# Kernel tuning notes

Hardware: AMD Instinct MI355X
Metric: run time of the kernel (lower is better)

## Reference

```python
import jax, jax.numpy as jnp
import numpy as np

B, T, H, DFF = 32, 4096, 512, 512  # hidden_size=512, d_ff=512, h feature dim = 2*H


def setup_inputs() -> dict:
    key = jax.random.key(0)
    ks = jax.random.split(key, 8)
    sc = 0.02
    return {
        "s": jax.random.normal(ks[0], (B, H), dtype=jnp.float32),
        "h": jax.random.normal(ks[1], (B, T, 2 * H), dtype=jnp.float32),
        "W_a_w": jax.random.normal(ks[2], (DFF, H), dtype=jnp.float32) * sc,
        "W_a_b": jnp.zeros((DFF,), dtype=jnp.float32),
        "U_a_w": jax.random.normal(ks[3], (DFF, 2 * H), dtype=jnp.float32) * sc,
        "U_a_b": jnp.zeros((DFF,), dtype=jnp.float32),
        "V_a_w": jax.random.normal(ks[4], (1, DFF), dtype=jnp.float32) * sc,
        "V_a_b": jnp.zeros((1,), dtype=jnp.float32),
    }


def reference(s, h, W_a_w, W_a_b, U_a_w, U_a_b, V_a_w, V_a_b):
    # Bahdanau additive attention scoring (NOTE: original has no softmax).
    ws = s @ W_a_w.T + W_a_b                              # [B, d_ff]
    uh = jnp.einsum('bte,fe->btf', h, U_a_w) + U_a_b       # [B, T, d_ff]
    x = jnp.tanh(ws[:, None, :] + uh)                      # [B, T, d_ff]
    energy = x @ V_a_w[0] + V_a_b[0]                       # [B, T]
    context = jnp.einsum('bt,bte->be', energy, h)          # [B, 2*hidden]
    return context
```

## Files before the change

kernel.cpp:

```cpp
#include <hip/hip_runtime.h>
#include <cstdint>
#include <cstddef>

#define B_SZ 32
#define T_SZ 4096
#define H2   1024
#define DFF_ 512
#define TM   64
#define NCHUNK 16
#define NSTEP 32

typedef __attribute__((ext_vector_type(8))) short bf16x8;
typedef __attribute__((ext_vector_type(4))) float f32x4;
typedef __attribute__((ext_vector_type(8))) unsigned short u16x8;

__device__ __forceinline__ unsigned short f2bf(float x) {
  unsigned u = __float_as_uint(x);
  u += 0x7fffu + ((u >> 16) & 1u);
  return (unsigned short)(u >> 16);
}

__device__ __forceinline__ void gll16(const float* g, void* l) {
  __builtin_amdgcn_global_load_lds(
      (const __attribute__((address_space(1))) unsigned int*)g,
      (__attribute__((address_space(3))) unsigned int*)l, 16, 0, 0);
}

__device__ __forceinline__ void memfence_sched() { asm volatile("" ::: "memory"); }

__device__ __forceinline__ void blk_barrier() {
  asm volatile("" ::: "memory");
  __builtin_amdgcn_s_barrier();
  asm volatile("" ::: "memory");
}

__global__ void prep_u_kernel(const float* __restrict__ U,
                              unsigned short* __restrict__ Upk) {
  int g = blockIdx.x * 256 + threadIdx.x;
  int j  = g & 7;
  int l  = (g >> 3) & 63;
  int ct = (g >> 9) & 31;
  int ks = g >> 14;
  int f  = ct * 16 + (l & 15);
  int k  = ks * 32 + (l >> 4) * 8 + j;
  Upk[g] = f2bf(U[f * H2 + k]);
}

__global__ void prep_ws_kernel(const float* __restrict__ s, const float* __restrict__ W,
                               const float* __restrict__ Wb, const float* __restrict__ Ub,
                               float* __restrict__ wsm) {
  int idx = blockIdx.x * 256 + threadIdx.x;
  int b = idx >> 9, f = idx & 511;
  const float4* s4 = (const float4*)(s + b * 512);
  const float4* w4 = (const float4*)(W + f * 512);
  float acc = 0.f;
  #pragma unroll 4
  for (int i = 0; i < 128; ++i) {
    float4 a = s4[i], w = w4[i];
    acc += a.x * w.x + a.y * w.y + a.z * w.z + a.w * w.w;
  }
  wsm[idx] = acc + Wb[f] + Ub[f];
}

__global__ __launch_bounds__(512, 4) void attn_main(
    const float* __restrict__ h, const unsigned short* __restrict__ Upk,
    const float* __restrict__ wsm, const float* __restrict__ Vw,
    const float* __restrict__ Vb, float* __restrict__ out) {
  __shared__ float F32c[2][4096];
  __shared__ unsigned short As16[2][4096];
  __shared__ float ws_s[DFF_];
  __shared__ float V_s[DFF_];
  __shared__ float energy_part[8][TM];
  __shared__ float energy_s[TM];

  const int tid  = threadIdx.x;
  const int blk  = blockIdx.x;
  const int b    = blk >> 6;
  const int t0   = (blk & 63) * TM;
  const int lane = tid & 63;
  const int wave = tid >> 6;
  const int ln15 = lane & 15;
  const int q4   = lane >> 4;

  ws_s[tid] = wsm[b * DFF_ + tid];
  V_s[tid]  = Vw[tid];

  const float* hbase = h + ((size_t)(b * T_SZ + t0)) * H2;

  const float* gsrc = hbase + (size_t)(8 * wave + (lane >> 4)) * H2 + (lane & 15) * 4;

  const int crow = 8 * wave + (lane >> 3);
  const int ckg  = lane & 7;
  const int cread  = crow * 64 + ckg * 8;
  const int cwrite = (ckg >> 2) * 2048 + (crow >> 4) * 512
                   + ((ckg & 3) * 16 + (crow & 15)) * 8;

  const bf16x8* Upk8 = (const bf16x8*)Upk;

  f32x4 acc[16];
  #pragma unroll
  for (int i = 0; i < 16; ++i) acc[i] = (f32x4){0.f, 0.f, 0.f, 0.f};
  bf16x8 bcur[8];

  gll16(gsrc,            (char*)&F32c[0][0] + wave * 2048);
  gll16(gsrc + 4 * H2,   (char*)&F32c[0][0] + wave * 2048 + 1024);
  memfence_sched();
  #pragma unroll
  for (int st = 0; st < 2; ++st)
    #pragma unroll
    for (int i = 0; i < 4; ++i)
      bcur[st * 4 + i] = Upk8[(size_t)(st * 32 + wave * 4 + i) * 64 + lane];
  memfence_sched();
  gll16(gsrc + 64,          (char*)&F32c[1][0] + wave * 2048);
  gll16(gsrc + 64 + 4 * H2, (char*)&F32c[1][0] + wave * 2048 + 1024);
  asm volatile("s_waitcnt vmcnt(10)" ::: "memory");
  {
    const float* src = &F32c[0][cread];
    float4 x0 = *(const float4*)src;
    float4 x1 = *(const float4*)(src + 4);
    u16x8 o;
    o[0] = f2bf(x0.x); o[1] = f2bf(x0.y); o[2] = f2bf(x0.z); o[3] = f2bf(x0.w);
    o[4] = f2bf(x1.x); o[5] = f2bf(x1.y); o[6] = f2bf(x1.z); o[7] = f2bf(x1.w);
    *(u16x8*)&As16[0][cwrite] = o;
  }
  blk_barrier();

  for (int c = 0; c < NCHUNK; ++c) {
    const unsigned short* Ab = &As16[c & 1][0];
    #pragma unroll
    for (int st = 0; st < 2; ++st) {
      #pragma unroll
      for (int rt = 0; rt < 4; ++rt) {
        bf16x8 af = *(const bf16x8*)&Ab[st * 2048 + rt * 512 + lane * 8];
        #pragma unroll
        for (int ct2 = 0; ct2 < 4; ++ct2)
          acc[ct2 * 4 + rt] =
            __builtin_amdgcn_mfma_f32_16x16x32_bf16(af, bcur[st * 4 + ct2],
                                                    acc[ct2 * 4 + rt], 0, 0, 0);
      }
    }
    if (c < NCHUNK - 1) {
      asm volatile("s_waitcnt vmcnt(0)" ::: "memory");
      {
        const float* src = &F32c[(c + 1) & 1][cread];
        float4 x0 = *(const float4*)src;
        float4 x1 = *(const float4*)(src + 4);
        u16x8 o;
        o[0] = f2bf(x0.x); o[1] = f2bf(x0.y); o[2] = f2bf(x0.z); o[3] = f2bf(x0.w);
        o[4] = f2bf(x1.x); o[5] = f2bf(x1.y); o[6] = f2bf(x1.z); o[7] = f2bf(x1.w);
        *(u16x8*)&As16[(c + 1) & 1][cwrite] = o;
      }
      blk_barrier();
      const int g0 = (c + 1) * 2;
      #pragma unroll
      for (int st = 0; st < 2; ++st)
        #pragma unroll
        for (int i = 0; i < 4; ++i)
          bcur[st * 4 + i] = Upk8[(size_t)((g0 + st) * 32 + wave * 4 + i) * 64 + lane];
      memfence_sched();
      if (c < NCHUNK - 2) {
        const float* gs = gsrc + (c + 2) * 64;
        char* ld = (char*)&F32c[c & 1][0] + wave * 2048;
        gll16(gs,          ld);
        gll16(gs + 4 * H2, ld + 1024);
      }
    }
  }

  float esum[16];
  #pragma unroll
  for (int i = 0; i < 16; ++i) esum[i] = 0.f;
  #pragma unroll
  for (int ct2 = 0; ct2 < 4; ++ct2) {
    int f = wave * 64 + ct2 * 16 + ln15;
    float wsf = ws_s[f], vf = V_s[f];
    #pragma unroll
    for (int rt = 0; rt < 4; ++rt) {
      #pragma unroll
      for (int rg = 0; rg < 4; ++rg) {
        float z = wsf + acc[ct2 * 4 + rt][rg];
        float e = __expf(2.f * z);
        float x = 1.f - 2.f / (e + 1.f);
        esum[rt * 4 + rg] += x * vf;
      }
    }
  }
  #pragma unroll
  for (int i = 0; i < 16; ++i) {
    #pragma unroll
    for (int m = 1; m < 16; m <<= 1) esum[i] += __shfl_xor(esum[i], m, 64);
  }
  if (ln15 == 0) {
    #pragma unroll
    for (int rt = 0; rt < 4; ++rt)
      #pragma unroll
      for (int rg = 0; rg < 4; ++rg)
        energy_part[wave][rt * 16 + q4 * 4 + rg] = esum[rt * 4 + rg];
  }
  __syncthreads();
  if (tid < TM) {
    float e = Vb[0];
    #pragma unroll
    for (int w = 0; w < 8; ++w) e += energy_part[w][tid];
    energy_s[tid] = e;
  }
  __syncthreads();

  int e0 = tid * 2;
  float c0 = 0.f, c1 = 0.f;
  const float2* h2p = (const float2*)hbase + (e0 >> 1);
  #pragma unroll 8
  for (int row = 0; row < TM; ++row) {
    float en = energy_s[row];
    float2 hv = h2p[(size_t)row * (H2 / 2)];
    c0 += en * hv.x;
    c1 += en * hv.y;
  }
  atomicAdd(&out[b * H2 + e0], c0);
  atomicAdd(&out[b * H2 + e0 + 1], c1);
}

extern "C" void kernel_launch(void* const* d_in, const int* in_sizes, int n_in,
                              void* d_out, int out_size, void* d_ws, size_t ws_size,
                              hipStream_t stream) {
  const float* s  = (const float*)d_in[0];
  const float* h  = (const float*)d_in[1];
  const float* Ww = (const float*)d_in[2];
  const float* Wb = (const float*)d_in[3];
  const float* Uw = (const float*)d_in[4];
  const float* Ub = (const float*)d_in[5];
  const float* Vw = (const float*)d_in[6];
  const float* Vb = (const float*)d_in[7];
  float* out = (float*)d_out;

  unsigned short* Upk = (unsigned short*)d_ws;
  float* wsm = (float*)((char*)d_ws + (size_t)NSTEP * 32768);

  hipMemsetAsync(out, 0, (size_t)out_size * sizeof(float), stream);
  prep_u_kernel<<<(DFF_ * H2) / 256, 256, 0, stream>>>(Uw, Upk);
  prep_ws_kernel<<<(B_SZ * DFF_) / 256, 256, 0, stream>>>(s, Ww, Wb, Ub, wsm);
  attn_main<<<B_SZ * (T_SZ / TM), 512, 0, stream>>>(h, Upk, wsm, Vw, Vb, out);
}
```

Measured before the change: 866.5 us.

## Triple-buffer h staging, reorder convert before MFMA, swizzle bf16 LDS tile

```diff
diff --git a/kernel.cpp b/kernel.cpp
--- a/kernel.cpp
+++ b/kernel.cpp
@@ -27,12 +27,6 @@
 }
 
 __device__ __forceinline__ void memfence_sched() { asm volatile("" ::: "memory"); }
-
-__device__ __forceinline__ void blk_barrier() {
-  asm volatile("" ::: "memory");
-  __builtin_amdgcn_s_barrier();
-  asm volatile("" ::: "memory");
-}
 
 __global__ void prep_u_kernel(const float* __restrict__ U,
                               unsigned short* __restrict__ Upk) {
@@ -66,7 +60,7 @@
     const float* __restrict__ h, const unsigned short* __restrict__ Upk,
     const float* __restrict__ wsm, const float* __restrict__ Vw,
     const float* __restrict__ Vb, float* __restrict__ out) {
-  __shared__ float F32c[2][4096];
+  __shared__ float F32c[3][4096];
   __shared__ unsigned short As16[2][4096];
   __shared__ float ws_s[DFF_];
   __shared__ float V_s[DFF_];
@@ -91,9 +85,11 @@
 
   const int crow = 8 * wave + (lane >> 3);
   const int ckg  = lane & 7;
-  const int cread  = crow * 64 + ckg * 8;
-  const int cwrite = (ckg >> 2) * 2048 + (crow >> 4) * 512
-                   + ((ckg & 3) * 16 + (crow & 15)) * 8;
+  const int cread = crow * 64 + ckg * 8;
+  int cwq = (ckg & 3) * 16 + (crow & 15);
+  cwq ^= (cwq >> 4) & 3;
+  const int cwrite = (ckg >> 2) * 2048 + (crow >> 4) * 512 + cwq * 8;
+  const int lrd = (lane ^ ((lane >> 4) & 3)) * 8;
 
   const bf16x8* Upk8 = (const bf16x8*)Upk;
 
@@ -102,8 +98,17 @@
   for (int i = 0; i < 16; ++i) acc[i] = (f32x4){0.f, 0.f, 0.f, 0.f};
   bf16x8 bcur[8];
 
-  gll16(gsrc,            (char*)&F32c[0][0] + wave * 2048);
-  gll16(gsrc + 4 * H2,   (char*)&F32c[0][0] + wave * 2048 + 1024);
+  {
+    char* lb = (char*)&F32c[0][0] + wave * 2048;
+    gll16(gsrc,          lb);
+    gll16(gsrc + 4 * H2, lb + 1024);
+    lb = (char*)&F32c[1][0] + wave * 2048;
+    gll16(gsrc + 64,          lb);
+    gll16(gsrc + 64 + 4 * H2, lb + 1024);
+    lb = (char*)&F32c[2][0] + wave * 2048;
+    gll16(gsrc + 128,          lb);
+    gll16(gsrc + 128 + 4 * H2, lb + 1024);
+  }
   memfence_sched();
   #pragma unroll
   for (int st = 0; st < 2; ++st)
@@ -111,9 +116,7 @@
     for (int i = 0; i < 4; ++i)
       bcur[st * 4 + i] = Upk8[(size_t)(st * 32 + wave * 4 + i) * 64 + lane];
   memfence_sched();
-  gll16(gsrc + 64,          (char*)&F32c[1][0] + wave * 2048);
-  gll16(gsrc + 64 + 4 * H2, (char*)&F32c[1][0] + wave * 2048 + 1024);
-  asm volatile("s_waitcnt vmcnt(10)" ::: "memory");
+  asm volatile("s_waitcnt vmcnt(12)" ::: "memory");
   {
     const float* src = &F32c[0][cread];
     float4 x0 = *(const float4*)src;
@@ -123,26 +126,18 @@
     o[4] = f2bf(x1.x); o[5] = f2bf(x1.y); o[6] = f2bf(x1.z); o[7] = f2bf(x1.w);
     *(u16x8*)&As16[0][cwrite] = o;
   }
-  blk_barrier();
-
+  asm volatile("s_waitcnt lgkmcnt(0)" ::: "memory");
+  __builtin_amdgcn_s_barrier();
+  memfence_sched();
+
+  int s0 = 0;
   for (int c = 0; c < NCHUNK; ++c) {
-    const unsigned short* Ab = &As16[c & 1][0];
-    #pragma unroll
-    for (int st = 0; st < 2; ++st) {
-      #pragma unroll
-      for (int rt = 0; rt < 4; ++rt) {
-        bf16x8 af = *(const bf16x8*)&Ab[st * 2048 + rt * 512 + lane * 8];
-        #pragma unroll
-        for (int ct2 = 0; ct2 < 4; ++ct2)
-          acc[ct2 * 4 + rt] =
-            __builtin_amdgcn_mfma_f32_16x16x32_bf16(af, bcur[st * 4 + ct2],
-                                                    acc[ct2 * 4 + rt], 0, 0, 0);
-      }
-    }
+    int s1 = s0 + 1; if (s1 == 3) s1 = 0;
     if (c < NCHUNK - 1) {
-      asm volatile("s_waitcnt vmcnt(0)" ::: "memory");
+      if (c < NCHUNK - 2) { asm volatile("s_waitcnt vmcnt(10)" ::: "memory"); }
+      else                { asm volatile("s_waitcnt vmcnt(8)"  ::: "memory"); }
       {
-        const float* src = &F32c[(c + 1) & 1][cread];
+        const float* src = &F32c[s1][cread];
         float4 x0 = *(const float4*)src;
         float4 x1 = *(const float4*)(src + 4);
         u16x8 o;
@@ -150,21 +145,39 @@
         o[4] = f2bf(x1.x); o[5] = f2bf(x1.y); o[6] = f2bf(x1.z); o[7] = f2bf(x1.w);
         *(u16x8*)&As16[(c + 1) & 1][cwrite] = o;
       }
-      blk_barrier();
+      if (c <= NCHUNK - 4) {
+        const float* gs = gsrc + (size_t)(c + 3) * 64;
+        char* lb = (char*)&F32c[s0][0] + wave * 2048;
+        gll16(gs,          lb);
+        gll16(gs + 4 * H2, lb + 1024);
+      }
+      memfence_sched();
+    }
+    const unsigned short* Ab = &As16[c & 1][0];
+    #pragma unroll
+    for (int st = 0; st < 2; ++st) {
+      #pragma unroll
+      for (int rt = 0; rt < 4; ++rt) {
+        bf16x8 af = *(const bf16x8*)&Ab[st * 2048 + rt * 512 + lrd];
+        #pragma unroll
+        for (int ct2 = 0; ct2 < 4; ++ct2)
+          acc[ct2 * 4 + rt] =
+            __builtin_amdgcn_mfma_f32_16x16x32_bf16(af, bcur[st * 4 + ct2],
+                                                    acc[ct2 * 4 + rt], 0, 0, 0);
+      }
+    }
+    if (c < NCHUNK - 1) {
       const int g0 = (c + 1) * 2;
       #pragma unroll
       for (int st = 0; st < 2; ++st)
         #pragma unroll
         for (int i = 0; i < 4; ++i)
           bcur[st * 4 + i] = Upk8[(size_t)((g0 + st) * 32 + wave * 4 + i) * 64 + lane];
+      asm volatile("s_waitcnt lgkmcnt(0)" ::: "memory");
+      __builtin_amdgcn_s_barrier();
       memfence_sched();
-      if (c < NCHUNK - 2) {
-        const float* gs = gsrc + (c + 2) * 64;
-        char* ld = (char*)&F32c[c & 1][0] + wave * 2048;
-        gll16(gs,          ld);
-        gll16(gs + 4 * H2, ld + 1024);
-      }
-    }
+    }
+    s0 = s1;
   }
 
   float esum[16];
```

Result: faster. 824.3 us (-4.9%).
